# Kernel optimization log

Measured on AMD Instinct MI355X. Metric: run time of the kernel, lower is better.

The kernel has to match this reference:

```python
import jax, jax.numpy as jnp
import numpy as np

N_LEVELS = 7
N_HEADS = 2
HIDDEN = 128
LP_P = 4.0  # LPPool1d norm


def setup_inputs() -> dict:
    key = jax.random.key(0)
    ks = jax.random.split(key, 9)
    B, S, H = 2048, 200, HIDDEN
    item_seq = jax.random.randint(ks[0], (B, S), 0, 100)
    item_seq_emb = jax.random.normal(ks[1], (B, S, H), dtype=jnp.float32)
    item_seq_len = jax.random.randint(ks[2], (B,), 0, S)
    scale = 0.02
    W_lq = jax.random.normal(ks[3], (H, H), dtype=jnp.float32) * scale
    b_lq = jnp.zeros((H,), dtype=jnp.float32)
    Wq = jax.random.normal(ks[4], (H, H), dtype=jnp.float32) * scale
    bq = jnp.zeros((H,), dtype=jnp.float32)
    Wk = jax.random.normal(ks[5], (H, H), dtype=jnp.float32) * scale
    bk = jnp.zeros((H,), dtype=jnp.float32)
    return {"item_seq": item_seq, "item_seq_emb": item_seq_emb,
            "item_seq_len": item_seq_len, "W_lq": W_lq, "b_lq": b_lq,
            "Wq": Wq, "bq": bq, "Wk": Wk, "bk": bk}


def reference(item_seq, item_seq_emb, item_seq_len, W_lq, b_lq, Wq, bq, Wk, bk):
    B, S, H = item_seq_emb.shape
    nh, L = N_HEADS, N_LEVELS
    d = H // nh
    mask = item_seq > 0  # [B,S]

    # multi-level gather of last j+1 positions; torch clamp(-1) + index -1 == last pos
    j = jnp.arange(L)
    idx = jnp.clip(item_seq_len[:, None] - (j[None, :] + 1), -1, 1000)  # [B,L]
    idx = jnp.where(idx < 0, idx + S, idx)
    gathered = jnp.take_along_axis(item_seq_emb, idx[:, :, None], axis=1)  # [B,L,H]
    level_emb = jnp.cumsum(gathered, axis=1)  # level i = sum of gathers 0..i

    # shared level-query linear (ModuleList([lin]*L) aliases one Linear)
    queries = level_emb @ W_lq.T + b_lq  # [B,L,H]

    # raw torch .view() reshapes replicated exactly
    q = (queries @ Wq.T + bq).reshape(B * nh, L, d)
    k = (item_seq_emb @ Wk.T + bk).reshape(B * nh, S, d)
    v = item_seq_emb.reshape(B, S, nh, d)

    alpha = jax.nn.sigmoid(jnp.einsum('bld,bsd->bls', q, k))  # [B*nh, L, S]
    alpha = alpha.reshape(B, nh * L, S).transpose(0, 2, 1)  # [B, S, nh*L]
    alpha = jax.nn.softmax(alpha, axis=1)

    # LPPool1d(p=4, kernel=L, stride=L) over last dim -> [B,S,nh]
    alpha = alpha.reshape(B, S, nh, L)
    alpha = jnp.sum(alpha ** LP_P, axis=-1) ** (1.0 / LP_P)

    alpha = jnp.where(mask[:, :, None], alpha, -jnp.inf)
    alpha = jax.nn.softmax(alpha, axis=1)  # dropout off (inference)

    weighted = (alpha[..., None] * v).reshape(B, S, H) * mask[:, :, None].astype(item_seq_emb.dtype)
    return jnp.sum(weighted, axis=1)  # [B,H]
```

## Files before the change

### kernel.cpp

```cpp
#include <hip/hip_runtime.h>
#include <hip/hip_bf16.h>

#define SEQ 200
#define HID 128
#define NLVL 7
#define ESTR 66

#define WS_M16_W 0
#define WS_BF    32768
#define WS_VB    33280
#define WS_CB    33792
#define WS_WC    33796
#define WS_BC    50180
#define WS_WORDS 50308

typedef __attribute__((ext_vector_type(8))) short short8;
typedef __attribute__((ext_vector_type(4))) float f32x4;

__device__ __forceinline__ float bf_lo(unsigned u) { return __uint_as_float(u << 16); }
__device__ __forceinline__ float bf_hi(unsigned u) { return __uint_as_float(u & 0xffff0000u); }
__device__ __forceinline__ unsigned short bf_bits(float f) {
    __hip_bfloat16 h = __float2bfloat16(f);
    return *reinterpret_cast<unsigned short*>(&h);
}
__device__ __forceinline__ unsigned pack_bf(float a, float b) {
    return (unsigned)bf_bits(a) | ((unsigned)bf_bits(b) << 16);
}

__global__ __launch_bounds__(256) void precomp0(
    const float* __restrict__ Wlq, const float* __restrict__ blq,
    const float* __restrict__ Wq,  const float* __restrict__ bq,
    float* __restrict__ ws)
{
    int id = blockIdx.x * 256 + threadIdx.x;
    int r = id >> 7, j = id & 127;
    float acc = 0.f;
    #pragma unroll 8
    for (int c = 0; c < 128; ++c) acc += Wq[r * 128 + c] * Wlq[c * 128 + j];
    ws[WS_WC + id] = acc;
    if (id < 128) {
        float b = bq[id];
        #pragma unroll 8
        for (int c = 0; c < 128; ++c) b += Wq[id * 128 + c] * blq[c];
        ws[WS_BC + id] = b;
    }
}

__global__ __launch_bounds__(256) void precomp1(
    const float* __restrict__ Wk, const float* __restrict__ bk, float* __restrict__ ws)
{
    int gid = blockIdx.x * 256 + threadIdx.x;
    if (gid < 65536) {
        int j = gid & 127, c = (gid >> 7) & 127, g = gid >> 14;
        int u = g >> 1, par = g & 1;
        const float* wc = ws + WS_WC + u * 64 * 128 + j;
        const float* wk = Wk + par * 64 * 128 + c;
        float acc = 0.f;
        #pragma unroll 8
        for (int d = 0; d < 64; ++d) acc += wc[d * 128] * wk[d * 128];
        ((__hip_bfloat16*)ws)[gid] = __float2bfloat16(acc);
    } else if (gid < 66048) {
        int t = gid - 65536, c = t & 127, g = t >> 7;
        int u = g >> 1, par = g & 1;
        float acc = 0.f;
        #pragma unroll 8
        for (int d = 0; d < 64; ++d)
            acc += ws[WS_BC + u * 64 + d] * Wk[(par * 64 + d) * 128 + c];
        ws[WS_BF + t] = acc;
    } else if (gid < 66560) {
        int t = gid - 66048, j = t & 127, g = t >> 7;
        int u = g >> 1, par = g & 1;
        float acc = 0.f;
        #pragma unroll 8
        for (int d = 0; d < 64; ++d)
            acc += ws[WS_WC + (u * 64 + d) * 128 + j] * bk[par * 64 + d];
        ws[WS_VB + t] = acc;
    } else if (gid < 66564) {
        int g = gid - 66560, u = g >> 1, par = g & 1;
        float acc = 0.f;
        for (int d = 0; d < 64; ++d)
            acc += ws[WS_BC + u * 64 + d] * bk[par * 64 + d];
        ws[WS_CB + g] = acc;
    }
}

__global__ __launch_bounds__(512, 4) void mixer_main(
    const int* __restrict__ item_seq,
    const float* __restrict__ emb,
    const int* __restrict__ seq_len,
    const float* __restrict__ ws,
    float* __restrict__ out)
{
    const int b   = blockIdx.x;
    const int tid = threadIdx.x;

    __shared__ __align__(16) unsigned s_embu[SEQ * ESTR];
    __shared__ __align__(16) float    s_qk[28 * 128];
    __shared__ float                  s_qb[28];
    __shared__ __align__(16) float    s_pool2[2800];
    __shared__ float                  s_A[2 * SEQ];
    __shared__ float                  s_inv[2];

    {
        const float4* src = (const float4*)(emb + (size_t)b * SEQ * HID);
        for (int i = tid; i < SEQ * 32; i += 512) {
            int row = i >> 5, j = i & 31;
            float4 v = src[i];
            unsigned* dst = s_embu + row * ESTR + 2 * j;
            dst[0] = pack_bf(v.x, v.y);
            dst[1] = pack_bf(v.z, v.w);
        }
    }
    if (tid < HID) {
        const int len = seq_len[b];
        const int c = tid;
        float e[NLVL];
        #pragma unroll
        for (int j = 0; j < NLVL; ++j) {
            int idx = len - (j + 1);
            if (idx < 0) idx = SEQ - 1;
            e[j] = emb[(size_t)b * SEQ * HID + (size_t)idx * HID + c];
        }
        short* lvl16 = (short*)(s_pool2 + 1024);
        float acc = 0.f;
        #pragma unroll
        for (int j = 0; j < NLVL; ++j) {
            acc += e[j];
            s_pool2[j * HID + c] = acc;
            lvl16[j * 136 + c] = (short)bf_bits(acc);
        }
    }
    __syncthreads();

    {
        const int w = tid >> 6, l = tid & 63;
        const int g = w >> 1, halfm = w & 1;
        const int mrow = l & 15, quad = l >> 4;
        const short* lvl16 = (const short*)(s_pool2 + 1024);
        short8 bfrag[4];
        #pragma unroll
        for (int k = 0; k < 4; ++k)
            bfrag[k] = *(const short8*)(lvl16 + mrow * 136 + k * 32 + quad * 8);
        const short* M16 = (const short*)ws;
        #pragma unroll
        for (int mt = 0; mt < 4; ++mt) {
            int mtile = halfm * 4 + mt;
            int cbase = mtile * 16 + quad * 4;
            f32x4 acc;
            #pragma unroll
            for (int r = 0; r < 4; ++r) acc[r] = ws[WS_BF + g * 128 + cbase + r];
            const short* Ab = M16 + (g * 128 + mtile * 16 + mrow) * 128;
            #pragma unroll
            for (int k = 0; k < 4; ++k) {
                short8 afrag = *(const short8*)(Ab + k * 32 + quad * 8);
                acc = __builtin_amdgcn_mfma_f32_16x16x32_bf16(afrag, bfrag[k], acc, 0, 0, 0);
            }
            if (mrow < NLVL)
                *(f32x4*)(s_qk + (mrow * 4 + g) * 128 + cbase) = acc;
        }
        if (tid < 28) {
            int qrow = tid, gg = qrow & 3, L = qrow >> 2;
            const float* vb = ws + WS_VB + gg * 128;
            const float* lv = s_pool2 + L * 128;
            float acc = ws[WS_CB + gg];
            #pragma unroll 8
            for (int j = 0; j < 128; ++j) acc += lv[j] * vb[j];
            s_qb[qrow] = acc;
        }
    }
    __syncthreads();

    for (int o = tid; o < 700; o += 512) {
        int hl = o / 50, gq = o % 50;
        int h = (hl >= 7) ? 1 : 0;
        int rA = h * 100 + gq, rB = rA + 50;
        const unsigned* eA = s_embu + rA * ESTR;
        const unsigned* eB = s_embu + rB * ESTR;
        const float4* k0 = (const float4*)(s_qk + (hl * 2) * 128);
        const float4* k1 = (const float4*)(s_qk + (hl * 2 + 1) * 128);
        float a0 = 0.f, a1 = 0.f, b0 = 0.f, b1 = 0.f;
        #pragma unroll 4
        for (int m = 0; m < 32; ++m) {
            uint2 ua = *(const uint2*)(eA + 2 * m);
            uint2 ub = *(const uint2*)(eB + 2 * m);
            float4 w0 = k0[m], w1 = k1[m];
            float x0 = bf_lo(ua.x), x1 = bf_hi(ua.x), x2 = bf_lo(ua.y), x3 = bf_hi(ua.y);
            float y0 = bf_lo(ub.x), y1 = bf_hi(ub.x), y2 = bf_lo(ub.y), y3 = bf_hi(ub.y);
            a0 += x0 * w0.x + x1 * w0.y + x2 * w0.z + x3 * w0.w;
            a1 += x0 * w1.x + x1 * w1.y + x2 * w1.z + x3 * w1.w;
            b0 += y0 * w0.x + y1 * w0.y + y2 * w0.z + y3 * w0.w;
            b1 += y0 * w1.x + y1 * w1.y + y2 * w1.z + y3 * w1.w;
        }
        float qb0 = s_qb[hl * 2], qb1 = s_qb[hl * 2 + 1];
        float* row = s_pool2 + hl * 200;
        *(float2*)(row + 2 * gq)       = make_float2(1.f / (1.f + __expf(-(a0 + qb0))),
                                                     1.f / (1.f + __expf(-(a1 + qb1))));
        *(float2*)(row + 2 * gq + 100) = make_float2(1.f / (1.f + __expf(-(b0 + qb0))),
                                                     1.f / (1.f + __expf(-(b1 + qb1))));
    }
    __syncthreads();

    const int wave = tid >> 6, lane = tid & 63;
    for (int r = wave; r < 14; r += 8) {
        float* row = s_pool2 + r * 200;
        float e0 = __expf(row[lane]);
        float e1 = __expf(row[lane + 64]);
        float e2 = __expf(row[lane + 128]);
        float e3 = (lane + 192 < 200) ? __expf(row[lane + 192]) : 0.f;
        float sum = e0 + e1 + e2 + e3;
        #pragma unroll
        for (int m = 1; m < 64; m <<= 1) sum += __shfl_xor(sum, m, 64);
        float inv = 1.f / sum;
        row[lane]       = e0 * inv;
        row[lane + 64]  = e1 * inv;
        row[lane + 128] = e2 * inv;
        if (lane + 192 < 200) row[lane + 192] = e3 * inv;
    }
    __syncthreads();

    if (tid < 2 * SEQ) {
        int h = tid / SEQ, s2 = tid % SEQ;
        float ssum = 0.f;
        #pragma unroll
        for (int l = 0; l < NLVL; ++l) {
            float v = s_pool2[(h * NLVL + l) * 200 + s2];
            float v2 = v * v;
            ssum += v2 * v2;
        }
        float A = sqrtf(sqrtf(ssum));
        int m = item_seq[(size_t)b * SEQ + s2];
        s_A[tid] = (m > 0) ? __expf(A) : 0.f;
    }
    __syncthreads();

    if (wave < 2) {
        const float* row = s_A + wave * SEQ;
        float sum = row[lane] + row[lane + 64] + row[lane + 128]
                  + ((lane + 192 < 200) ? row[lane + 192] : 0.f);
        #pragma unroll
        for (int m = 1; m < 64; m <<= 1) sum += __shfl_xor(sum, m, 64);
        if (lane == 0) s_inv[wave] = 1.f / sum;
    }
    __syncthreads();

    {
        int c = tid & 127, qq = tid >> 7;
        int h = c >> 6;
        const float* wv = s_A + h * SEQ + qq * 50;
        const unsigned* eb = s_embu + (qq * 50) * ESTR + (c >> 1);
        float acc = 0.f;
        #pragma unroll 5
        for (int s = 0; s < 50; ++s) {
            unsigned u = eb[s * ESTR];
            acc += wv[s] * ((c & 1) ? bf_hi(u) : bf_lo(u));
        }
        s_qk[tid] = acc;
    }
    __syncthreads();
    if (tid < HID) {
        int h = tid >> 6;
        float tot = (s_qk[tid] + s_qk[tid + 128] + s_qk[tid + 256] + s_qk[tid + 384]) * s_inv[h];
        out[(size_t)b * HID + tid] = tot;
    }
}

__global__ __launch_bounds__(256) void mixer_fallback(
    const int* __restrict__ item_seq, const float* __restrict__ emb,
    const int* __restrict__ seq_len,
    const float* __restrict__ Wlq, const float* __restrict__ blq,
    const float* __restrict__ Wq,  const float* __restrict__ bq,
    const float* __restrict__ Wk,  const float* __restrict__ bk,
    float* __restrict__ out)
{
    const int b = blockIdx.x, tid = threadIdx.x;
    __shared__ unsigned s_embu[SEQ * 65];
    __shared__ float s_qk[28 * 128];
    __shared__ float s_qb[28];
    __shared__ float s_tmp[2800];
    __shared__ float s_A[400];
    __shared__ float s_red[256];
    __shared__ float s_inv[2];

    {
        const float4* src = (const float4*)(emb + (size_t)b * SEQ * HID);
        for (int i = tid; i < SEQ * 32; i += 256) {
            int row = i >> 5, j = i & 31;
            float4 v = src[i];
            unsigned* dst = s_embu + row * 65 + 2 * j;
            dst[0] = pack_bf(v.x, v.y);
            dst[1] = pack_bf(v.z, v.w);
        }
    }
    const int len = seq_len[b];
    if (tid < HID) {
        float acc = 0.f;
        for (int j = 0; j < NLVL; ++j) {
            int idx = len - (j + 1);
            if (idx < 0) idx = SEQ - 1;
            acc += emb[(size_t)b * SEQ * HID + (size_t)idx * HID + tid];
            s_tmp[j * HID + tid] = acc;
        }
    }
    __syncthreads();
    for (int t = tid; t < NLVL * HID; t += 256) {
        int l = t >> 7, c = t & 127;
        const float* x = s_tmp + l * HID;
        float acc = blq[c];
        #pragma unroll 8
        for (int k = 0; k < HID; ++k) acc += x[k] * Wlq[c * HID + k];
        s_tmp[896 + t] = acc;
    }
    __syncthreads();
    for (int t = tid; t < NLVL * HID; t += 256) {
        int l = t >> 7, c = t & 127;
        const float* x = s_tmp + 896 + l * HID;
        float acc = bq[c];
        #pragma unroll 8
        for (int k = 0; k < HID; ++k) acc += x[k] * Wq[c * HID + k];
        s_tmp[t] = acc;
    }
    __syncthreads();
    for (int o = tid; o < 28 * 128; o += 256) {
        int qrow = o >> 7, c = o & 127;
        int hl = qrow >> 1, par = qrow & 1;
        const float* qv = s_tmp + hl * 64;
        float acc = 0.f;
        #pragma unroll 8
        for (int d2 = 0; d2 < 64; ++d2) acc += qv[d2] * Wk[(par * 64 + d2) * HID + c];
        s_qk[qrow * 128 + c] = acc;
    }
    if (tid < 28) {
        int hl = tid >> 1, par = tid & 1;
        float acc = 0.f;
        for (int d2 = 0; d2 < 64; ++d2) acc += s_tmp[hl * 64 + d2] * bk[par * 64 + d2];
        s_qb[tid] = acc;
    }
    __syncthreads();
    for (int o = tid; o < 700; o += 256) {
        int hl = o / 50, g = o % 50;
        int h = (hl >= 7) ? 1 : 0;
        int rA = h * 100 + g, rB = rA + 50;
        const unsigned* eA = s_embu + rA * 65;
        const unsigned* eB = s_embu + rB * 65;
        const float* k0 = s_qk + (hl * 2) * 128;
        const float* k1 = s_qk + (hl * 2 + 1) * 128;
        float a0 = 0.f, a1 = 0.f, c0a = 0.f, c1a = 0.f;
        #pragma unroll 4
        for (int kk = 0; kk < 64; ++kk) {
            unsigned uA = eA[kk], uB = eB[kk];
            float2 w0 = *(const float2*)(k0 + 2 * kk);
            float2 w1 = *(const float2*)(k1 + 2 * kk);
            float alo = bf_lo(uA), ahi = bf_hi(uA);
            float blo = bf_lo(uB), bhi = bf_hi(uB);
            a0 += alo * w0.x + ahi * w0.y;  a1 += alo * w1.x + ahi * w1.y;
            c0a += blo * w0.x + bhi * w0.y; c1a += blo * w1.x + bhi * w1.y;
        }
        float qb0 = s_qb[hl * 2], qb1 = s_qb[hl * 2 + 1];
        float* row = s_tmp + hl * 200;
        row[2 * g]       = 1.f / (1.f + __expf(-(a0 + qb0)));
        row[2 * g + 1]   = 1.f / (1.f + __expf(-(a1 + qb1)));
        row[2 * g + 100] = 1.f / (1.f + __expf(-(c0a + qb0)));
        row[2 * g + 101] = 1.f / (1.f + __expf(-(c1a + qb1)));
    }
    __syncthreads();
    const int wave = tid >> 6, lane = tid & 63;
    for (int r = wave; r < 14; r += 4) {
        float* row = s_tmp + r * 200;
        float e0 = __expf(row[lane]), e1 = __expf(row[lane + 64]);
        float e2 = __expf(row[lane + 128]);
        float e3 = (lane + 192 < 200) ? __expf(row[lane + 192]) : 0.f;
        float sum = e0 + e1 + e2 + e3;
        #pragma unroll
        for (int m = 1; m < 64; m <<= 1) sum += __shfl_xor(sum, m, 64);
        float inv = 1.f / sum;
        row[lane] = e0 * inv; row[lane + 64] = e1 * inv; row[lane + 128] = e2 * inv;
        if (lane + 192 < 200) row[lane + 192] = e3 * inv;
    }
    __syncthreads();
    for (int o = tid; o < 2 * SEQ; o += 256) {
        int h = o / SEQ, s2 = o % SEQ;
        float ssum = 0.f;
        #pragma unroll
        for (int l = 0; l < NLVL; ++l) {
            float v = s_tmp[(h * NLVL + l) * 200 + s2];
            float v2 = v * v; ssum += v2 * v2;
        }
        float A = sqrtf(sqrtf(ssum));
        s_A[o] = (item_seq[(size_t)b * SEQ + s2] > 0) ? __expf(A) : 0.f;
    }
    __syncthreads();
    if (wave < 2) {
        const float* row = s_A + wave * SEQ;
        float sum = row[lane] + row[lane + 64] + row[lane + 128]
                  + ((lane + 192 < 200) ? row[lane + 192] : 0.f);
        #pragma unroll
        for (int m = 1; m < 64; m <<= 1) sum += __shfl_xor(sum, m, 64);
        if (lane == 0) s_inv[wave] = 1.f / sum;
    }
    __syncthreads();
    {
        int c = tid & 127, halfb = tid >> 7;
        int h = c >> 6;
        const float* wv = s_A + h * SEQ + halfb * 100;
        float acc = 0.f;
        #pragma unroll 4
        for (int s2 = 0; s2 < 100; ++s2) {
            unsigned u = s_embu[(halfb * 100 + s2) * 65 + (c >> 1)];
            acc += wv[s2] * ((c & 1) ? bf_hi(u) : bf_lo(u));
        }
        s_red[tid] = acc;
    }
    __syncthreads();
    if (tid < HID) {
        int h = tid >> 6;
        out[(size_t)b * HID + tid] = (s_red[tid] + s_red[tid + 128]) * s_inv[h];
    }
}

extern "C" void kernel_launch(void* const* d_in, const int* in_sizes, int n_in,
                              void* d_out, int out_size, void* d_ws, size_t ws_size,
                              hipStream_t stream) {
    const int* item_seq = (const int*)d_in[0];
    const float* emb    = (const float*)d_in[1];
    const int* seq_len  = (const int*)d_in[2];
    const float* Wlq    = (const float*)d_in[3];
    const float* blq    = (const float*)d_in[4];
    const float* Wq     = (const float*)d_in[5];
    const float* bq     = (const float*)d_in[6];
    const float* Wk     = (const float*)d_in[7];
    const float* bk     = (const float*)d_in[8];
    float* out          = (float*)d_out;
    const int B = in_sizes[2];

    if (ws_size >= (size_t)WS_WORDS * 4) {
        float* ws = (float*)d_ws;
        precomp0<<<64, 256, 0, stream>>>(Wlq, blq, Wq, bq, ws);
        precomp1<<<261, 256, 0, stream>>>(Wk, bk, ws);
        mixer_main<<<B, 512, 0, stream>>>(item_seq, emb, seq_len, ws, out);
    } else {
        mixer_fallback<<<B, 256, 0, stream>>>(item_seq, emb, seq_len, Wlq, blq, Wq, bq, Wk, bk, out);
    }
}
```

Before: 392.2 us.

## Drop LDS embedding staging; compute scores with split-bf16 MFMA from global

The per-block bf16 copy of the embedding in shared memory is removed. Attention scores are now computed with MFMA, reading embedding rows straight from global memory and splitting the query-key vectors into hi/lo bf16 parts to keep precision. The final weighted sum also reads fp32 embeddings from global memory, and the softmax normalisations are folded into later stages to drop two barriers. The much smaller LDS footprint allows raising launch bounds to 8 blocks per CU, at the cost of re-reading the embedding from global or L2 twice per block instead of once.

```diff
diff --git a/kernel.cpp b/kernel.cpp
--- a/kernel.cpp
+++ b/kernel.cpp
@@ -4,7 +4,6 @@
 #define SEQ 200
 #define HID 128
 #define NLVL 7
-#define ESTR 66
 
 #define WS_M16_W 0
 #define WS_BF    32768
@@ -84,63 +83,61 @@
     }
 }
 
-__global__ __launch_bounds__(512, 4) void mixer_main(
+__global__ __launch_bounds__(512, 8) void mixer_main(
     const int* __restrict__ item_seq,
     const float* __restrict__ emb,
     const int* __restrict__ seq_len,
     const float* __restrict__ ws,
     float* __restrict__ out)
 {
-    const int b   = blockIdx.x;
-    const int tid = threadIdx.x;
-
-    __shared__ __align__(16) unsigned s_embu[SEQ * ESTR];
-    __shared__ __align__(16) float    s_qk[28 * 128];
-    __shared__ float                  s_qb[28];
-    __shared__ __align__(16) float    s_pool2[2800];
-    __shared__ float                  s_A[2 * SEQ];
-    __shared__ float                  s_inv[2];
-
-    {
-        const float4* src = (const float4*)(emb + (size_t)b * SEQ * HID);
-        for (int i = tid; i < SEQ * 32; i += 512) {
-            int row = i >> 5, j = i & 31;
-            float4 v = src[i];
-            unsigned* dst = s_embu + row * ESTR + 2 * j;
-            dst[0] = pack_bf(v.x, v.y);
-            dst[1] = pack_bf(v.z, v.w);
-        }
-    }
+    const int b    = blockIdx.x;
+    const int tid  = threadIdx.x;
+    const int wave = tid >> 6, lane = tid & 63;
+
+    __shared__ __align__(16) short s_qkhi[30 * 136];
+    __shared__ __align__(16) short s_qklo[30 * 136];
+    __shared__ __align__(16) char  s_region[14 * 208 * 4];
+    __shared__ float s_qb[28];
+    __shared__ float s_rinv[14];
+    __shared__ __align__(16) float s_A[2 * SEQ];
+    __shared__ __align__(16) float s_red[512];
+
+    float* s_scores = (float*)s_region;
+    float* s_lvl    = (float*)s_region;
+    short* s_lvl16  = (short*)(s_region + 3584);
+
+    const float* embb = emb + (size_t)b * SEQ * HID;
+
     if (tid < HID) {
         const int len = seq_len[b];
-        const int c = tid;
         float e[NLVL];
         #pragma unroll
         for (int j = 0; j < NLVL; ++j) {
             int idx = len - (j + 1);
             if (idx < 0) idx = SEQ - 1;
-            e[j] = emb[(size_t)b * SEQ * HID + (size_t)idx * HID + c];
-        }
-        short* lvl16 = (short*)(s_pool2 + 1024);
+            e[j] = embb[(size_t)idx * HID + tid];
+        }
         float acc = 0.f;
         #pragma unroll
         for (int j = 0; j < NLVL; ++j) {
             acc += e[j];
-            s_pool2[j * HID + c] = acc;
-            lvl16[j * 136 + c] = (short)bf_bits(acc);
-        }
+            s_lvl[j * HID + tid] = acc;
+            s_lvl16[j * 136 + tid] = (short)bf_bits(acc);
+        }
+    } else if (tid < 196) {
+        int t = tid - 128;
+        ((uint2*)(s_qkhi + 28 * 136))[t] = make_uint2(0u, 0u);
+        ((uint2*)(s_qklo + 28 * 136))[t] = make_uint2(0u, 0u);
     }
     __syncthreads();
 
     {
-        const int w = tid >> 6, l = tid & 63;
-        const int g = w >> 1, halfm = w & 1;
-        const int mrow = l & 15, quad = l >> 4;
-        const short* lvl16 = (const short*)(s_pool2 + 1024);
+        const int g = wave >> 1, halfm = wave & 1;
+        const int mrow = lane & 15, quad = lane >> 4;
         short8 bfrag[4];
         #pragma unroll
         for (int k = 0; k < 4; ++k)
-            bfrag[k] = *(const short8*)(lvl16 + mrow * 136 + k * 32 + quad * 8);
+            bfrag[k] = *(const short8*)(s_lvl16 + mrow * 136 + k * 32 + quad * 8);
         const short* M16 = (const short*)ws;
         #pragma unroll
         for (int mt = 0; mt < 4; ++mt) {
@@ -155,13 +152,20 @@
                 short8 afrag = *(const short8*)(Ab + k * 32 + quad * 8);
                 acc = __builtin_amdgcn_mfma_f32_16x16x32_bf16(afrag, bfrag[k], acc, 0, 0, 0);
             }
-            if (mrow < NLVL)
-                *(f32x4*)(s_qk + (mrow * 4 + g) * 128 + cbase) = acc;
+            if (mrow < NLVL) {
+                int qrow = mrow * 4 + g;
+                unsigned h01 = pack_bf(acc[0], acc[1]);
+                unsigned h23 = pack_bf(acc[2], acc[3]);
+                float l0 = acc[0] - bf_lo(h01), l1 = acc[1] - bf_hi(h01);
+                float l2 = acc[2] - bf_lo(h23), l3 = acc[3] - bf_hi(h23);
+                *(uint2*)(s_qkhi + qrow * 136 + cbase) = make_uint2(h01, h23);
+                *(uint2*)(s_qklo + qrow * 136 + cbase) = make_uint2(pack_bf(l0, l1), pack_bf(l2, l3));
+            }
         }
         if (tid < 28) {
             int qrow = tid, gg = qrow & 3, L = qrow >> 2;
             const float* vb = ws + WS_VB + gg * 128;
-            const float* lv = s_pool2 + L * 128;
+            const float* lv = s_lvl + L * 128;
             float acc = ws[WS_CB + gg];
             #pragma unroll 8
             for (int j = 0; j < 128; ++j) acc += lv[j] * vb[j];
@@ -170,51 +174,56 @@
     }
     __syncthreads();
 
-    for (int o = tid; o < 700; o += 512) {
-        int hl = o / 50, gq = o % 50;
-        int h = (hl >= 7) ? 1 : 0;
-        int rA = h * 100 + gq, rB = rA + 50;
-        const unsigned* eA = s_embu + rA * ESTR;
-        const unsigned* eB = s_embu + rB * ESTR;
-        const float4* k0 = (const float4*)(s_qk + (hl * 2) * 128);
-        const float4* k1 = (const float4*)(s_qk + (hl * 2 + 1) * 128);
-        float a0 = 0.f, a1 = 0.f, b0 = 0.f, b1 = 0.f;
-        #pragma unroll 4
-        for (int m = 0; m < 32; ++m) {
-            uint2 ua = *(const uint2*)(eA + 2 * m);
-            uint2 ub = *(const uint2*)(eB + 2 * m);
-            float4 w0 = k0[m], w1 = k1[m];
-            float x0 = bf_lo(ua.x), x1 = bf_hi(ua.x), x2 = bf_lo(ua.y), x3 = bf_hi(ua.y);
-            float y0 = bf_lo(ub.x), y1 = bf_hi(ub.x), y2 = bf_lo(ub.y), y3 = bf_hi(ub.y);
-            a0 += x0 * w0.x + x1 * w0.y + x2 * w0.z + x3 * w0.w;
-            a1 += x0 * w1.x + x1 * w1.y + x2 * w1.z + x3 * w1.w;
-            b0 += y0 * w0.x + y1 * w0.y + y2 * w0.z + y3 * w0.w;
-            b1 += y0 * w1.x + y1 * w1.y + y2 * w1.z + y3 * w1.w;
-        }
-        float qb0 = s_qb[hl * 2], qb1 = s_qb[hl * 2 + 1];
-        float* row = s_pool2 + hl * 200;
-        *(float2*)(row + 2 * gq)       = make_float2(1.f / (1.f + __expf(-(a0 + qb0))),
-                                                     1.f / (1.f + __expf(-(a1 + qb1))));
-        *(float2*)(row + 2 * gq + 100) = make_float2(1.f / (1.f + __expf(-(b0 + qb0))),
-                                                     1.f / (1.f + __expf(-(b1 + qb1))));
-    }
-    __syncthreads();
-
-    const int wave = tid >> 6, lane = tid & 63;
-    for (int r = wave; r < 14; r += 8) {
-        float* row = s_pool2 + r * 200;
+    {
+        const int ln = lane & 15, quad = lane >> 4;
+        #pragma unroll 1
+        for (int t = wave; t < 14; t += 8) {
+            const int h = t / 7, mtile = t % 7;
+            int gqrow = mtile * 16 + ln;
+            int rowg = h * 100 + (gqrow < 100 ? gqrow : 99);
+            const float* Arow = embb + (size_t)rowg * HID;
+            float qbv = (ln < 14) ? s_qb[h * 14 + ln] : 0.f;
+            f32x4 acc;
+            acc[0] = qbv; acc[1] = qbv; acc[2] = qbv; acc[3] = qbv;
+            #pragma unroll 2
+            for (int kk = 0; kk < 4; ++kk) {
+                float4 v0 = *(const float4*)(Arow + kk * 32 + quad * 8);
+                float4 v1 = *(const float4*)(Arow + kk * 32 + quad * 8 + 4);
+                short8 afrag;
+                afrag[0] = (short)bf_bits(v0.x); afrag[1] = (short)bf_bits(v0.y);
+                afrag[2] = (short)bf_bits(v0.z); afrag[3] = (short)bf_bits(v0.w);
+                afrag[4] = (short)bf_bits(v1.x); afrag[5] = (short)bf_bits(v1.y);
+                afrag[6] = (short)bf_bits(v1.z); afrag[7] = (short)bf_bits(v1.w);
+                const int boff = (h * 14 + ln) * 136 + kk * 32 + quad * 8;
+                short8 bhi = *(const short8*)(s_qkhi + boff);
+                short8 blo = *(const short8*)(s_qklo + boff);
+                acc = __builtin_amdgcn_mfma_f32_16x16x32_bf16(afrag, bhi, acc, 0, 0, 0);
+                acc = __builtin_amdgcn_mfma_f32_16x16x32_bf16(afrag, blo, acc, 0, 0, 0);
+            }
+            if (ln < 14) {
+                int srow = (h * 7 + (ln >> 1)) * 208;
+                int par = ln & 1;
+                #pragma unroll
+                for (int i = 0; i < 4; ++i) {
+                    int gq = mtile * 16 + quad * 4 + i;
+                    if (gq < 100)
+                        s_scores[srow + 2 * gq + par] = 1.f / (1.f + __expf(-acc[i]));
+                }
+            }
+        }
+    }
+    __syncthreads();
+
+    for (int rr = wave; rr < 14; rr += 8) {
+        const float* row = s_scores + rr * 208;
         float e0 = __expf(row[lane]);
         float e1 = __expf(row[lane + 64]);
         float e2 = __expf(row[lane + 128]);
         float e3 = (lane + 192 < 200) ? __expf(row[lane + 192]) : 0.f;
         float sum = e0 + e1 + e2 + e3;
         #pragma unroll
-        for (int m = 1; m < 64; m <<= 1) sum += __shfl_xor(sum, m, 64);
-        float inv = 1.f / sum;
-        row[lane]       = e0 * inv;
-        row[lane + 64]  = e1 * inv;
-        row[lane + 128] = e2 * inv;
-        if (lane + 192 < 200) row[lane + 192] = e3 * inv;
+        for (int mm = 1; mm < 64; mm <<= 1) sum += __shfl_xor(sum, mm, 64);
+        if (lane == 0) s_rinv[rr] = 1.f / sum;
     }
     __syncthreads();
 
@@ -223,23 +232,13 @@
         float ssum = 0.f;
         #pragma unroll
         for (int l = 0; l < NLVL; ++l) {
-            float v = s_pool2[(h * NLVL + l) * 200 + s2];
+            float v = __expf(s_scores[(h * NLVL + l) * 208 + s2]) * s_rinv[h * NLVL + l];
             float v2 = v * v;
             ssum += v2 * v2;
         }
         float A = sqrtf(sqrtf(ssum));
         int m = item_seq[(size_t)b * SEQ + s2];
         s_A[tid] = (m > 0) ? __expf(A) : 0.f;
-    }
-    __syncthreads();
-
-    if (wave < 2) {
-        const float* row = s_A + wave * SEQ;
-        float sum = row[lane] + row[lane + 64] + row[lane + 128]
-                  + ((lane + 192 < 200) ? row[lane + 192] : 0.f);
-        #pragma unroll
-        for (int m = 1; m < 64; m <<= 1) sum += __shfl_xor(sum, m, 64);
-        if (lane == 0) s_inv[wave] = 1.f / sum;
     }
     __syncthreads();
 
@@ -247,19 +246,24 @@
         int c = tid & 127, qq = tid >> 7;
         int h = c >> 6;
         const float* wv = s_A + h * SEQ + qq * 50;
-        const unsigned* eb = s_embu + (qq * 50) * ESTR + (c >> 1);
-        float acc = 0.f;
-        #pragma unroll 5
-        for (int s = 0; s < 50; ++s) {
-            unsigned u = eb[s * ESTR];
-            acc += wv[s] * ((c & 1) ? bf_hi(u) : bf_lo(u));
-        }
-        s_qk[tid] = acc;
-    }
-    __syncthreads();
+        const float* eg = embb + (size_t)(qq * 50) * HID + c;
+        float acc = 0.f;
+        #pragma unroll 10
+        for (int s = 0; s < 50; ++s)
+            acc += wv[s] * eg[(size_t)s * HID];
+        s_red[tid] = acc;
+    }
+    __syncthreads();
+
     if (tid < HID) {
         int h = tid >> 6;
-        float tot = (s_qk[tid] + s_qk[tid + 128] + s_qk[tid + 256] + s_qk[tid + 384]) * s_inv[h];
+        const float* row = s_A + h * SEQ;
+        float sum = row[lane] + row[lane + 64] + row[lane + 128]
+                  + ((lane + 192 < 200) ? row[lane + 192] : 0.f);
+        #pragma unroll
+        for (int mm = 1; mm < 64; mm <<= 1) sum += __shfl_xor(sum, mm, 64);
+        float inv = 1.f / sum;
+        float tot = (s_red[tid] + s_red[tid + 128] + s_red[tid + 256] + s_red[tid + 384]) * inv;
         out[(size_t)b * HID + tid] = tot;
     }
 }
```

Result: faster. 358.8 us (-8.5%).
